# Kernel optimization log

Hardware: AMD Instinct MI355X
Metric: run time of the kernel (lower is better)

Reference implementation:

```python
import jax, jax.numpy as jnp
import numpy as np

B_, L_, DM_, DS_, DC_, EXP_ = 2, 2048, 1024, 16, 4, 2
DI_ = EXP_ * DM_

def setup_inputs() -> dict:
    key = jax.random.key(0)
    ks = jax.random.split(key, 8)
    rn = lambda k, shape, s: (jax.random.normal(k, shape, dtype=jnp.float32) * s)
    return {
        "x": rn(ks[0], (B_, L_, DM_), 1.0),
        "in_proj_w": rn(ks[1], (2 * DI_, DM_), 0.02),
        "conv_w": rn(ks[2], (DI_, 1, DC_), 0.1),
        "conv_b": jnp.zeros((DI_,), dtype=jnp.float32),
        "x_proj_w": rn(ks[3], (2 * DS_ + 1, DI_), 0.02),
        "dt_proj_w": rn(ks[4], (DI_, 1), 0.02),
        "dt_proj_b": jnp.full((DI_,), -2.0, dtype=jnp.float32),
        "A_log": rn(ks[5], (DI_, DS_), 1.0),
        "D": jnp.ones((DI_,), dtype=jnp.float32),
        "out_proj_w": rn(ks[6], (DM_, DI_), 0.02),
    }


def reference(x, in_proj_w, conv_w, conv_b, x_proj_w, dt_proj_w, dt_proj_b, A_log, D, out_proj_w):
    b, l, dm = x.shape
    di, ds = A_log.shape
    dc = conv_w.shape[-1]

    # in_proj -> split into u (ssm stream) and z (gate)
    xz = x @ in_proj_w.T                      # (b, l, 2*di)
    u, z = xz[..., :di], xz[..., di:]

    # causal depthwise conv1d (torch pads both sides then slices [:l] == left pad only)
    uc = jnp.transpose(u, (0, 2, 1))          # (b, di, l)
    uc = jax.lax.conv_general_dilated(
        uc, conv_w, window_strides=(1,), padding=[(dc - 1, 0)],
        feature_group_count=di, dimension_numbers=("NCH", "OIH", "NCH"))
    uc = uc + conv_b[None, :, None]
    u = jnp.transpose(uc, (0, 2, 1)) * jax.nn.silu(z)   # (b, l, di)

    # input-dependent SSM params
    proj = u @ x_proj_w.T                     # (b, l, 2*ds + 1)
    delta = proj[..., :1]                     # (b, l, 1)
    Bm = proj[..., 1:1 + ds]                  # (b, l, ds)
    Cm = proj[..., 1 + ds:]                   # (b, l, ds)
    delta = jax.nn.softplus(delta @ dt_proj_w.T + dt_proj_b)  # (b, l, di)

    A = -jnp.exp(A_log)                       # (di, ds)

    def step(h, inp):
        ut, dt, Bt, Ct = inp                  # (b,di) (b,di) (b,ds) (b,ds)
        dte = jnp.exp(dt)                     # faithful to source: exp(softplus(...))
        A_bar = jnp.exp(A[None] * dte[..., None])          # (b, di, ds)
        h = A_bar * h + (Bt[:, None, :] * dte[..., None]) * ut[..., None]
        yt = jnp.einsum("bis,bs->bi", h, Ct) + D * ut
        return h, yt

    h0 = jnp.zeros((b, di, ds), dtype=x.dtype)
    xs = (jnp.transpose(u, (1, 0, 2)), jnp.transpose(delta, (1, 0, 2)),
          jnp.transpose(Bm, (1, 0, 2)), jnp.transpose(Cm, (1, 0, 2)))
    _, ys = jax.lax.scan(step, h0, xs)        # ys: (l, b, di)
    y = jnp.transpose(ys, (1, 0, 2))          # (b, l, di)
    return y @ out_proj_w.T                   # (b, l, dm)
```

## Files before the change

### kernel.cpp

```cpp
#include <hip/hip_runtime.h>
#include <hip/hip_bf16.h>
#include <cstddef>
#include <cstdint>

#define B_N 2
#define L_N 2048
#define DM_N 1024
#define DS_N 16
#define DI_N 2048
#define NTOK (B_N * L_N)
#define NPROJ 33
#define NPJ 36
#define NC 32
#define CL (L_N / NC)
#define XKC 8
#define XKCL (DI_N / XKC)

typedef __attribute__((ext_vector_type(8))) short short8v;
typedef __attribute__((ext_vector_type(4))) float f32x4;
typedef __attribute__((address_space(1))) void av1;
typedef __attribute__((address_space(3))) void av3;

__device__ __forceinline__ void gload16(const void* g, void* l) {
  __builtin_amdgcn_global_load_lds((av1*)g, (av3*)l, 16, 0, 0);
}

__device__ __forceinline__ unsigned short f2bf_rn(float f) {
  uint32_t u = __float_as_uint(f);
  uint32_t r = (u + 0x7fffu + ((u >> 16) & 1u)) >> 16;
  return (unsigned short)r;
}
__device__ __forceinline__ float bf2f(unsigned short h) {
  return __uint_as_float((uint32_t)h << 16);
}

__global__ __launch_bounds__(256) void split_pack_kernel(
    const float* __restrict__ src, uint32_t* __restrict__ dst, int n8) {
  int idx = blockIdx.x * 256 + threadIdx.x;
  if (idx >= n8) return;
  const float4* s = (const float4*)src + (size_t)idx * 2;
  float4 v0 = s[0], v1 = s[1];
  float f[8] = {v0.x, v0.y, v0.z, v0.w, v1.x, v1.y, v1.z, v1.w};
  uint32_t hi[4], lo[4];
#pragma unroll
  for (int j = 0; j < 4; ++j) {
    unsigned short h0 = f2bf_rn(f[2 * j]);
    unsigned short h1 = f2bf_rn(f[2 * j + 1]);
    unsigned short l0 = f2bf_rn(f[2 * j] - bf2f(h0));
    unsigned short l1 = f2bf_rn(f[2 * j + 1] - bf2f(h1));
    hi[j] = (uint32_t)h0 | ((uint32_t)h1 << 16);
    lo[j] = (uint32_t)l0 | ((uint32_t)l1 << 16);
  }
  uint4* d = (uint4*)dst + (size_t)idx * 2;
  d[0] = make_uint4(hi[0], hi[1], hi[2], hi[3]);
  d[1] = make_uint4(lo[0], lo[1], lo[2], lo[3]);
}

__global__ __launch_bounds__(256) void gemm_pk_nt(
    const char* __restrict__ Apk, const char* __restrict__ Bpk,
    float* __restrict__ C, int N, int K4, int gx) {
  __shared__ __align__(16) char lds[32768];
  const int tid = threadIdx.x;
  const int lane = tid & 63;
  const int wave = tid >> 6;

  const int nwg = gridDim.x;
  const int cpx = nwg >> 3;
  const int bid = blockIdx.x;
  const int wg = (bid & 7) * cpx + (bid >> 3);
  const int bx = wg % gx;
  const int by = wg / gx;
  const int m0 = by * 128, n0 = bx * 128;

  const int wr = wave >> 1, wc = wave & 1;

  const char* gbase = (wave & 2) ? Bpk : Apk;
  const int rowbase = ((wave & 2) ? n0 : m0) + (wave & 1) * 64;
  const int rloc = lane >> 3;
  const int sslot = (lane & 7) ^ rloc;
  const char* gsrc = gbase + (size_t)(rowbase + rloc) * K4 + sslot * 16;
  const size_t cstride = (size_t)8 * K4;
  char* ldst = lds + wave * 8192 + lane * 16;

  f32x4 acc[4][4] = {};
  const int fr = lane & 15;
  const int fg = lane >> 4;
  const int sA = ((fg * 2) ^ (fr & 7)) * 16;
  const int abase = (wr * 64 + fr) * 128 + sA;
  const int bbase = 16384 + (wc * 64 + fr) * 128 + sA;

  for (int kt4 = 0; kt4 < K4; kt4 += 128) {
#pragma unroll
    for (int c = 0; c < 8; ++c)
      gload16(gsrc + c * cstride + kt4, ldst + c * 1024);
    __syncthreads();

    short8v afh[4], afl[4], bfh[4], bfl[4];
#pragma unroll
    for (int m = 0; m < 4; ++m) {
      int a = abase + m * 2048;
      afh[m] = *(const short8v*)(lds + a);
      afl[m] = *(const short8v*)(lds + (a ^ 16));
    }
#pragma unroll
    for (int n = 0; n < 4; ++n) {
      int b = bbase + n * 2048;
      bfh[n] = *(const short8v*)(lds + b);
      bfl[n] = *(const short8v*)(lds + (b ^ 16));
    }
#pragma unroll
    for (int m = 0; m < 4; ++m) {
#pragma unroll
      for (int n = 0; n < 4; ++n) {
        asm("v_mfma_f32_16x16x32_bf16 %0, %1, %2, %0"
            : "+v"(acc[m][n]) : "v"(afh[m]), "v"(bfh[n]));
        asm("v_mfma_f32_16x16x32_bf16 %0, %1, %2, %0"
            : "+v"(acc[m][n]) : "v"(afh[m]), "v"(bfl[n]));
        asm("v_mfma_f32_16x16x32_bf16 %0, %1, %2, %0"
            : "+v"(acc[m][n]) : "v"(afl[m]), "v"(bfh[n]));
      }
    }
    __syncthreads();
  }

#pragma unroll
  for (int m = 0; m < 4; ++m) {
#pragma unroll
    for (int n = 0; n < 4; ++n) {
#pragma unroll
      for (int q = 0; q < 4; ++q) {
        int row = m0 + wr * 64 + m * 16 + fg * 4 + q;
        int col = n0 + wc * 64 + n * 16 + fr;
        C[(size_t)row * N + col] = acc[m][n][q];
      }
    }
  }
}

__global__ __launch_bounds__(256) void conv_silu_kernel(
    const float* __restrict__ xz, const float* __restrict__ cw,
    const float* __restrict__ cb, float* __restrict__ u2) {
  size_t idx = (size_t)blockIdx.x * 256 + threadIdx.x;
  if (idx >= (size_t)NTOK * DI_N) return;
  int i = (int)(idx & (DI_N - 1));
  int n = (int)(idx >> 11);
  int l = n & (L_N - 1);
  const float* base = xz + (size_t)n * (2 * DI_N) + i;
  const float4 w = *(const float4*)&cw[i * 4];
  float acc = fmaf(w.w, base[0], cb[i]);
  if (l >= 1) acc = fmaf(w.z, base[-(ptrdiff_t)(2 * DI_N)], acc);
  if (l >= 2) acc = fmaf(w.y, base[-(ptrdiff_t)(4 * DI_N)], acc);
  if (l >= 3) acc = fmaf(w.x, base[-(ptrdiff_t)(6 * DI_N)], acc);
  float z = base[DI_N];
  float sil = z / (1.f + __expf(-z));
  u2[(size_t)n * DI_N + i] = acc * sil;
}

__global__ __launch_bounds__(256) void xproj_part_kernel(
    const float* __restrict__ u2, const float* __restrict__ xw,
    float* __restrict__ part) {
  __shared__ float uS[16][257];
  __shared__ float wS[33][257];
  const int tid = threadIdx.x;
  const int kc = blockIdx.x & (XKC - 1);
  const int rb = blockIdx.x >> 3;
  const int row0 = rb * 16;
  const int k0 = kc * XKCL;

#pragma unroll
  for (int it = 0; it < 4; ++it) {
    int slot = tid + it * 256;
    int r = slot >> 6;
    int kq = (slot & 63) << 2;
    float4 v = *(const float4*)&u2[(size_t)(row0 + r) * DI_N + k0 + kq];
    uS[r][kq] = v.x; uS[r][kq + 1] = v.y;
    uS[r][kq + 2] = v.z; uS[r][kq + 3] = v.w;
  }
#pragma unroll
  for (int it = 0; it < 9; ++it) {
    int slot = tid + it * 256;
    if (slot < 33 * 64) {
      int c = slot >> 6;
      int kq = (slot & 63) << 2;
      float4 v = *(const float4*)&xw[(size_t)c * DI_N + k0 + kq];
      wS[c][kq] = v.x; wS[c][kq + 1] = v.y;
      wS[c][kq + 2] = v.z; wS[c][kq + 3] = v.w;
    }
  }
  __syncthreads();

  const int r = tid & 15;
  const int cg = tid >> 4;
  const int c0 = cg * 3;
  const int rc0 = c0 > 32 ? 32 : c0;
  const int rc1 = c0 + 1 > 32 ? 32 : c0 + 1;
  const int rc2 = c0 + 2 > 32 ? 32 : c0 + 2;
  float a0 = 0.f, a1 = 0.f, a2 = 0.f;
#pragma unroll 4
  for (int k = 0; k < XKCL; ++k) {
    float uv = uS[r][k];
    a0 = fmaf(uv, wS[rc0][k], a0);
    a1 = fmaf(uv, wS[rc1][k], a1);
    a2 = fmaf(uv, wS[rc2][k], a2);
  }
  size_t base = (size_t)kc * (NTOK * NPJ) + (size_t)(row0 + r) * NPJ;
  if (c0 < NPROJ)     part[base + (c0 == 0 ? 0 : c0 + 3)] = a0;
  if (c0 + 1 < NPROJ) part[base + c0 + 4] = a1;
  if (c0 + 2 < NPROJ) part[base + c0 + 5] = a2;
}

__global__ __launch_bounds__(256) void xproj_reduce_kernel(
    const float* __restrict__ part, float* __restrict__ proj) {
  int idx = blockIdx.x * 256 + threadIdx.x;
  float s = 0.f;
#pragma unroll
  for (int kc = 0; kc < XKC; ++kc)
    s += part[(size_t)kc * (NTOK * NPJ) + idx];
  proj[idx] = s;
}

__global__ __launch_bounds__(256) void scan_pass1_kernel(
    const float* __restrict__ u2, const float* __restrict__ pj,
    const float* __restrict__ dtw, const float* __restrict__ dtb,
    const float* __restrict__ A_log,
    float* __restrict__ carryH, float* __restrict__ carryP) {
  const int t = blockIdx.x * 256 + threadIdx.x;
  const int i = t & (DI_N - 1);
  const int rest = t >> 11;
  const int c = rest & (NC - 1);
  const int b = rest >> 5;
  const float LOG2E = 1.4426950408889634f;

  float A2[16];
#pragma unroll
  for (int q = 0; q < 4; ++q) {
    float4 v = *(const float4*)&A_log[i * DS_N + q * 4];
    A2[q * 4 + 0] = -__expf(v.x) * LOG2E;
    A2[q * 4 + 1] = -__expf(v.y) * LOG2E;
    A2[q * 4 + 2] = -__expf(v.z) * LOG2E;
    A2[q * 4 + 3] = -__expf(v.w) * LOG2E;
  }
  const float wl = dtw[i] * LOG2E;
  const float bl = dtb[i] * LOG2E;

  float h[16] = {};
  float sdte = 0.f;
  const int l0 = c * CL;
  const float* un = u2 + ((size_t)b * L_N + l0) * DI_N + i;
  const float* pr = pj + ((size_t)b * L_N + l0) * NPJ;

#pragma unroll 2
  for (int l = 0; l < CL; ++l) {
    float uv = un[(size_t)l * DI_N];
    const float* row = pr + l * NPJ;
    float d0 = row[0];
    float4 B0 = *(const float4*)(row + 4);
    float4 B1 = *(const float4*)(row + 8);
    float4 B2 = *(const float4*)(row + 12);
    float4 B3 = *(const float4*)(row + 16);
    float dte = 1.f + exp2f(fmaf(d0, wl, bl));
    float du = dte * uv;
    sdte += dte;
    float Bv[16] = {B0.x, B0.y, B0.z, B0.w, B1.x, B1.y, B1.z, B1.w,
                    B2.x, B2.y, B2.z, B2.w, B3.x, B3.y, B3.z, B3.w};
#pragma unroll
    for (int s = 0; s < 16; ++s) {
      float a = exp2f(A2[s] * dte);
      h[s] = fmaf(a, h[s], Bv[s] * du);
    }
  }
  size_t cbase = (((size_t)c * B_N + b) * DI_N + i) * DS_N;
#pragma unroll
  for (int q = 0; q < 4; ++q) {
    float4 hv = {h[q * 4], h[q * 4 + 1], h[q * 4 + 2], h[q * 4 + 3]};
    *(float4*)&carryH[cbase + q * 4] = hv;
    float4 pv = {exp2f(A2[q * 4] * sdte), exp2f(A2[q * 4 + 1] * sdte),
                 exp2f(A2[q * 4 + 2] * sdte), exp2f(A2[q * 4 + 3] * sdte)};
    *(float4*)&carryP[cbase + q * 4] = pv;
  }
}

__global__ __launch_bounds__(256) void scan_fixup_kernel(
    float* __restrict__ carryH, const float* __restrict__ carryP) {
  const int q = blockIdx.x * 256 + threadIdx.x;
  float h = 0.f;
#pragma unroll 4
  for (int c = 0; c < NC; ++c) {
    size_t idx = (size_t)c * (B_N * DI_N * DS_N) + q;
    float Hc = carryH[idx];
    float Pc = carryP[idx];
    carryH[idx] = h;
    h = fmaf(Pc, h, Hc);
  }
}

__global__ __launch_bounds__(256) void scan_pass2_kernel(
    const float* __restrict__ u2, const float* __restrict__ pj,
    const float* __restrict__ dtw, const float* __restrict__ dtb,
    const float* __restrict__ A_log, const float* __restrict__ Dp,
    const float* __restrict__ carryH, char* __restrict__ ypk) {
  const int t = blockIdx.x * 256 + threadIdx.x;
  const int i = t & (DI_N - 1);
  const int rest = t >> 11;
  const int c = rest & (NC - 1);
  const int b = rest >> 5;
  const float LOG2E = 1.4426950408889634f;

  float A2[16];
#pragma unroll
  for (int q = 0; q < 4; ++q) {
    float4 v = *(const float4*)&A_log[i * DS_N + q * 4];
    A2[q * 4 + 0] = -__expf(v.x) * LOG2E;
    A2[q * 4 + 1] = -__expf(v.y) * LOG2E;
    A2[q * 4 + 2] = -__expf(v.z) * LOG2E;
    A2[q * 4 + 3] = -__expf(v.w) * LOG2E;
  }
  const float wl = dtw[i] * LOG2E;
  const float bl = dtb[i] * LOG2E;
  const float Dd = Dp[i];

  float h[16];
  size_t cbase = (((size_t)c * B_N + b) * DI_N + i) * DS_N;
#pragma unroll
  for (int q = 0; q < 4; ++q) {
    float4 hv = *(const float4*)&carryH[cbase + q * 4];
    h[q * 4] = hv.x; h[q * 4 + 1] = hv.y;
    h[q * 4 + 2] = hv.z; h[q * 4 + 3] = hv.w;
  }

  const int l0 = c * CL;
  const float* un = u2 + ((size_t)b * L_N + l0) * DI_N + i;
  const float* pr = pj + ((size_t)b * L_N + l0) * NPJ;
  char* yb = ypk + ((size_t)b * L_N + l0) * (DI_N * 4) + (i >> 3) * 32 + (i & 7) * 2;

#pragma unroll 2
  for (int l = 0; l < CL; ++l) {
    float uv = un[(size_t)l * DI_N];
    const float* row = pr + l * NPJ;
    float d0 = row[0];
    float4 B0 = *(const float4*)(row + 4);
    float4 B1 = *(const float4*)(row + 8);
    float4 B2 = *(const float4*)(row + 12);
    float4 B3 = *(const float4*)(row + 16);
    float4 C0 = *(const float4*)(row + 20);
    float4 C1 = *(const float4*)(row + 24);
    float4 C2 = *(const float4*)(row + 28);
    float4 C3 = *(const float4*)(row + 32);
    float dte = 1.f + exp2f(fmaf(d0, wl, bl));
    float du = dte * uv;
    float Bv[16] = {B0.x, B0.y, B0.z, B0.w, B1.x, B1.y, B1.z, B1.w,
                    B2.x, B2.y, B2.z, B2.w, B3.x, B3.y, B3.z, B3.w};
    float Cv[16] = {C0.x, C0.y, C0.z, C0.w, C1.x, C1.y, C1.z, C1.w,
                    C2.x, C2.y, C2.z, C2.w, C3.x, C3.y, C3.z, C3.w};
    float y = Dd * uv;
#pragma unroll
    for (int s = 0; s < 16; ++s) {
      float a = exp2f(A2[s] * dte);
      h[s] = fmaf(a, h[s], Bv[s] * du);
      y = fmaf(h[s], Cv[s], y);
    }
    unsigned short hh = f2bf_rn(y);
    char* q = yb + (size_t)l * (DI_N * 4);
    *(unsigned short*)q = hh;
    *(unsigned short*)(q + 16) = f2bf_rn(y - bf2f(hh));
  }
}

extern "C" void kernel_launch(void* const* d_in, const int* in_sizes, int n_in,
                              void* d_out, int out_size, void* d_ws, size_t ws_size,
                              hipStream_t stream) {
  const float* x          = (const float*)d_in[0];
  const float* in_proj_w  = (const float*)d_in[1];
  const float* conv_w     = (const float*)d_in[2];
  const float* conv_b     = (const float*)d_in[3];
  const float* x_proj_w   = (const float*)d_in[4];
  const float* dt_proj_w  = (const float*)d_in[5];
  const float* dt_proj_b  = (const float*)d_in[6];
  const float* A_log      = (const float*)d_in[7];
  const float* Dp         = (const float*)d_in[8];
  const float* out_proj_w = (const float*)d_in[9];
  float* out = (float*)d_out;

  char* ws = (char*)d_ws;
  float* xz = (float*)ws;
  float* u2 = (float*)(ws + (size_t)NTOK * 2 * DI_N * 4);

  char* x_pk  = (char*)u2;
  char* w1_pk = x_pk + (size_t)NTOK * DM_N * 4;

  char*  y_pk   = ws;
  float* carryH = (float*)(ws + 33554432);
  float* carryP = (float*)(ws + 41943040);
  char*  w2_pk  = ws + 50331648;
  float* xpart  = (float*)(ws + 58720256);
  float* proj36 = (float*)(ws + 63438848);

  {
    int n8 = NTOK * DM_N / 8;
    split_pack_kernel<<<n8 / 256, 256, 0, stream>>>(x, (uint32_t*)x_pk, n8);
    split_pack_kernel<<<n8 / 256, 256, 0, stream>>>(in_proj_w, (uint32_t*)w1_pk, n8);
  }
  gemm_pk_nt<<<1024, 256, 0, stream>>>(x_pk, w1_pk, xz, 2 * DI_N, DM_N * 4, 32);
  {
    int nblk = (int)(((size_t)NTOK * DI_N + 255) / 256);
    conv_silu_kernel<<<nblk, 256, 0, stream>>>(xz, conv_w, conv_b, u2);
  }
  {
    int n8 = DM_N * DI_N / 8;
    split_pack_kernel<<<n8 / 256, 256, 0, stream>>>(out_proj_w, (uint32_t*)w2_pk, n8);
  }
  {
    xproj_part_kernel<<<(NTOK / 16) * XKC, 256, 0, stream>>>(u2, x_proj_w, xpart);
    xproj_reduce_kernel<<<(NTOK * NPJ) / 256, 256, 0, stream>>>(xpart, proj36);
  }
  {
    int nblk = (B_N * DI_N * NC) / 256;
    scan_pass1_kernel<<<nblk, 256, 0, stream>>>(u2, proj36, dt_proj_w, dt_proj_b,
                                                A_log, carryH, carryP);
    scan_fixup_kernel<<<(B_N * DI_N * DS_N) / 256, 256, 0, stream>>>(carryH, carryP);
    scan_pass2_kernel<<<nblk, 256, 0, stream>>>(u2, proj36, dt_proj_w, dt_proj_b,
                                                A_log, Dp, carryH, y_pk);
  }
  gemm_pk_nt<<<256, 256, 0, stream>>>(y_pk, w2_pk, out, DM_N, DI_N * 4, 8);
}
```

Baseline: 434.2 us.

## Double scan chunks, stage projection rows in LDS, store chunk dt sums

```diff
diff --git a/kernel.cpp b/kernel.cpp
--- a/kernel.cpp
+++ b/kernel.cpp
@@ -11,7 +11,7 @@
 #define NTOK (B_N * L_N)
 #define NPROJ 33
 #define NPJ 36
-#define NC 32
+#define NC 64
 #define CL (L_N / NC)
 #define XKC 8
 #define XKCL (DI_N / XKC)
@@ -223,13 +223,22 @@
     const float* __restrict__ u2, const float* __restrict__ pj,
     const float* __restrict__ dtw, const float* __restrict__ dtb,
     const float* __restrict__ A_log,
-    float* __restrict__ carryH, float* __restrict__ carryP) {
-  const int t = blockIdx.x * 256 + threadIdx.x;
-  const int i = t & (DI_N - 1);
-  const int rest = t >> 11;
-  const int c = rest & (NC - 1);
-  const int b = rest >> 5;
+    float* __restrict__ carryH, float* __restrict__ sdteO) {
+  __shared__ float pS[CL][20];
+  const int tid = threadIdx.x;
+  const int bid = blockIdx.x;
+  const int ib = bid & 7;
+  const int c = (bid >> 3) & (NC - 1);
+  const int b = bid >> 9;
+  const int i = ib * 256 + tid;
+  const int l0 = c * CL;
   const float LOG2E = 1.4426950408889634f;
+
+  if (tid < CL * 5) {
+    int row = tid / 5, j = tid % 5;
+    float4 v = *(const float4*)&pj[((size_t)b * L_N + l0 + row) * NPJ + j * 4];
+    *(float4*)&pS[row][j * 4] = v;
+  }
 
   float A2[16];
 #pragma unroll
@@ -242,24 +251,22 @@
   }
   const float wl = dtw[i] * LOG2E;
   const float bl = dtb[i] * LOG2E;
+  const float* un = u2 + ((size_t)b * L_N + l0) * DI_N + i;
+  __syncthreads();
 
   float h[16] = {};
   float sdte = 0.f;
-  const int l0 = c * CL;
-  const float* un = u2 + ((size_t)b * L_N + l0) * DI_N + i;
-  const float* pr = pj + ((size_t)b * L_N + l0) * NPJ;
-
+  float ucur = un[0];
 #pragma unroll 2
   for (int l = 0; l < CL; ++l) {
-    float uv = un[(size_t)l * DI_N];
-    const float* row = pr + l * NPJ;
-    float d0 = row[0];
-    float4 B0 = *(const float4*)(row + 4);
-    float4 B1 = *(const float4*)(row + 8);
-    float4 B2 = *(const float4*)(row + 12);
-    float4 B3 = *(const float4*)(row + 16);
+    float unext = (l + 1 < CL) ? un[(size_t)(l + 1) * DI_N] : 0.f;
+    float d0 = pS[l][0];
+    float4 B0 = *(const float4*)&pS[l][4];
+    float4 B1 = *(const float4*)&pS[l][8];
+    float4 B2 = *(const float4*)&pS[l][12];
+    float4 B3 = *(const float4*)&pS[l][16];
     float dte = 1.f + exp2f(fmaf(d0, wl, bl));
-    float du = dte * uv;
+    float du = dte * ucur;
     sdte += dte;
     float Bv[16] = {B0.x, B0.y, B0.z, B0.w, B1.x, B1.y, B1.z, B1.w,
                     B2.x, B2.y, B2.z, B2.w, B3.x, B3.y, B3.z, B3.w};
@@ -268,29 +275,33 @@
       float a = exp2f(A2[s] * dte);
       h[s] = fmaf(a, h[s], Bv[s] * du);
     }
+    ucur = unext;
   }
   size_t cbase = (((size_t)c * B_N + b) * DI_N + i) * DS_N;
 #pragma unroll
   for (int q = 0; q < 4; ++q) {
     float4 hv = {h[q * 4], h[q * 4 + 1], h[q * 4 + 2], h[q * 4 + 3]};
     *(float4*)&carryH[cbase + q * 4] = hv;
-    float4 pv = {exp2f(A2[q * 4] * sdte), exp2f(A2[q * 4 + 1] * sdte),
-                 exp2f(A2[q * 4 + 2] * sdte), exp2f(A2[q * 4 + 3] * sdte)};
-    *(float4*)&carryP[cbase + q * 4] = pv;
-  }
+  }
+  sdteO[((size_t)c * B_N + b) * DI_N + i] = sdte;
 }
 
 __global__ __launch_bounds__(256) void scan_fixup_kernel(
-    float* __restrict__ carryH, const float* __restrict__ carryP) {
+    float* __restrict__ carryH, const float* __restrict__ sdte,
+    const float* __restrict__ A_log) {
   const int q = blockIdx.x * 256 + threadIdx.x;
+  const int s = q & 15;
+  const int i = (q >> 4) & (DI_N - 1);
+  const float LOG2E = 1.4426950408889634f;
+  const float A2 = -__expf(A_log[i * DS_N + s]) * LOG2E;
   float h = 0.f;
-#pragma unroll 4
+#pragma unroll 8
   for (int c = 0; c < NC; ++c) {
     size_t idx = (size_t)c * (B_N * DI_N * DS_N) + q;
     float Hc = carryH[idx];
-    float Pc = carryP[idx];
+    float sd = sdte[(size_t)c * (B_N * DI_N) + (q >> 4)];
     carryH[idx] = h;
-    h = fmaf(Pc, h, Hc);
+    h = fmaf(exp2f(A2 * sd), h, Hc);
   }
 }
 
@@ -299,12 +310,25 @@
     const float* __restrict__ dtw, const float* __restrict__ dtb,
     const float* __restrict__ A_log, const float* __restrict__ Dp,
     const float* __restrict__ carryH, char* __restrict__ ypk) {
-  const int t = blockIdx.x * 256 + threadIdx.x;
-  const int i = t & (DI_N - 1);
-  const int rest = t >> 11;
-  const int c = rest & (NC - 1);
-  const int b = rest >> 5;
+  __shared__ float pS[CL][36];
+  const int tid = threadIdx.x;
+  const int bid = blockIdx.x;
+  const int ib = bid & 7;
+  const int c = (bid >> 3) & (NC - 1);
+  const int b = bid >> 9;
+  const int i = ib * 256 + tid;
+  const int l0 = c * CL;
   const float LOG2E = 1.4426950408889634f;
+
+#pragma unroll
+  for (int it = 0; it < 2; ++it) {
+    int slot = tid + it * 256;
+    if (slot < CL * 9) {
+      int row = slot / 9, j = slot % 9;
+      float4 v = *(const float4*)&pj[((size_t)b * L_N + l0 + row) * NPJ + j * 4];
+      *(float4*)&pS[row][j * 4] = v;
+    }
+  }
 
   float A2[16];
 #pragma unroll
@@ -328,31 +352,30 @@
     h[q * 4 + 2] = hv.z; h[q * 4 + 3] = hv.w;
   }
 
-  const int l0 = c * CL;
   const float* un = u2 + ((size_t)b * L_N + l0) * DI_N + i;
-  const float* pr = pj + ((size_t)b * L_N + l0) * NPJ;
   char* yb = ypk + ((size_t)b * L_N + l0) * (DI_N * 4) + (i >> 3) * 32 + (i & 7) * 2;
-
+  __syncthreads();
+
+  float ucur = un[0];
 #pragma unroll 2
   for (int l = 0; l < CL; ++l) {
-    float uv = un[(size_t)l * DI_N];
-    const float* row = pr + l * NPJ;
-    float d0 = row[0];
-    float4 B0 = *(const float4*)(row + 4);
-    float4 B1 = *(const float4*)(row + 8);
-    float4 B2 = *(const float4*)(row + 12);
-    float4 B3 = *(const float4*)(row + 16);
-    float4 C0 = *(const float4*)(row + 20);
-    float4 C1 = *(const float4*)(row + 24);
-    float4 C2 = *(const float4*)(row + 28);
-    float4 C3 = *(const float4*)(row + 32);
+    float unext = (l + 1 < CL) ? un[(size_t)(l + 1) * DI_N] : 0.f;
+    float d0 = pS[l][0];
+    float4 B0 = *(const float4*)&pS[l][4];
+    float4 B1 = *(const float4*)&pS[l][8];
+    float4 B2 = *(const float4*)&pS[l][12];
+    float4 B3 = *(const float4*)&pS[l][16];
+    float4 C0 = *(const float4*)&pS[l][20];
+    float4 C1 = *(const float4*)&pS[l][24];
+    float4 C2 = *(const float4*)&pS[l][28];
+    float4 C3 = *(const float4*)&pS[l][32];
     float dte = 1.f + exp2f(fmaf(d0, wl, bl));
-    float du = dte * uv;
+    float du = dte * ucur;
     float Bv[16] = {B0.x, B0.y, B0.z, B0.w, B1.x, B1.y, B1.z, B1.w,
                     B2.x, B2.y, B2.z, B2.w, B3.x, B3.y, B3.z, B3.w};
     float Cv[16] = {C0.x, C0.y, C0.z, C0.w, C1.x, C1.y, C1.z, C1.w,
                     C2.x, C2.y, C2.z, C2.w, C3.x, C3.y, C3.z, C3.w};
-    float y = Dd * uv;
+    float y = Dd * ucur;
 #pragma unroll
     for (int s = 0; s < 16; ++s) {
       float a = exp2f(A2[s] * dte);
@@ -363,6 +386,7 @@
     char* q = yb + (size_t)l * (DI_N * 4);
     *(unsigned short*)q = hh;
     *(unsigned short*)(q + 16) = f2bf_rn(y - bf2f(hh));
+    ucur = unext;
   }
 }
 
@@ -390,10 +414,10 @@
 
   char*  y_pk   = ws;
   float* carryH = (float*)(ws + 33554432);
-  float* carryP = (float*)(ws + 41943040);
-  char*  w2_pk  = ws + 50331648;
-  float* xpart  = (float*)(ws + 58720256);
-  float* proj36 = (float*)(ws + 63438848);
+  float* sdte   = (float*)(ws + 50331648);
+  char*  w2_pk  = ws + 51380224;
+  float* xpart  = (float*)(ws + 59768832);
+  float* proj36 = (float*)(ws + 64487424);
 
   {
     int n8 = NTOK * DM_N / 8;
@@ -414,10 +438,11 @@
     xproj_reduce_kernel<<<(NTOK * NPJ) / 256, 256, 0, stream>>>(xpart, proj36);
   }
   {
-    int nblk = (B_N * DI_N * NC) / 256;
+    int nblk = B_N * NC * (DI_N / 256);
     scan_pass1_kernel<<<nblk, 256, 0, stream>>>(u2, proj36, dt_proj_w, dt_proj_b,
-                                                A_log, carryH, carryP);
-    scan_fixup_kernel<<<(B_N * DI_N * DS_N) / 256, 256, 0, stream>>>(carryH, carryP);
+                                                A_log, carryH, sdte);
+    scan_fixup_kernel<<<(B_N * DI_N * DS_N) / 256, 256, 0, stream>>>(carryH, sdte,
+                                                                     A_log);
     scan_pass2_kernel<<<nblk, 256, 0, stream>>>(u2, proj36, dt_proj_w, dt_proj_b,
                                                 A_log, Dp, carryH, y_pk);
   }
```

After: 369.8 us. 14.8% less time.
